# Kernel optimization log

Hardware: AMD Instinct MI355X
Metric: run time of the kernel (lower is better)

## Reference

```python
import jax, jax.numpy as jnp
import numpy as np

KERNEL_SIZE = 2
DILATION = 2


def aconv(x, A, shift):
    # x: [n, c, v, l], A: [v, w]; temporal roll + zero-mask first `shift` steps,
    # then node diffusion x . A over the node axis.
    xr = jnp.roll(x, shift, axis=3)
    if shift > 0:
        xr = xr.at[..., :shift].set(0.0)
    return jnp.einsum('ncvl,vw->ncwl', xr, A)


def setup_inputs() -> dict:
    key = jax.random.key(0)
    ks = jax.random.split(key, 7)
    N, C, V, L, E, CO = 32, 64, 500, 64, 10, 64
    return {
        'x': jax.random.normal(ks[0], (N, C, V, L), dtype=jnp.float32),
        'nodevec1': jax.random.normal(ks[1], (V, E), dtype=jnp.float32),
        'nodevec2': jax.random.normal(ks[2], (E, V), dtype=jnp.float32),
        'et_w': jax.random.normal(ks[3], (E, E), dtype=jnp.float32),
        'et_b': jax.random.normal(ks[4], (E,), dtype=jnp.float32),
        'mlp_w': jax.random.normal(ks[5], (CO, (1 + KERNEL_SIZE) * C), dtype=jnp.float32) * 0.05,
        'mlp_b': jax.random.normal(ks[6], (CO,), dtype=jnp.float32),
    }


def reference(x, nodevec1, nodevec2, et_w, et_b, mlp_w, mlp_b):
    out = [x]
    x2 = x
    shift = 0
    # hop 0: adaptive adjacency from node embeddings
    adp = jax.nn.softmax(jax.nn.relu(nodevec1 @ nodevec2), axis=1)
    x1 = aconv(x2, adp, shift)
    out.append(x1)
    shift = DILATION
    x2 = x1
    for i in range(KERNEL_SIZE - 1):
        # emb_trans: affine update of both node embeddings
        nodevec1 = nodevec1 @ et_w + et_b
        nodevec2 = (nodevec2.T @ et_w + et_b).T
        adp = jax.nn.softmax(jax.nn.relu(nodevec1 @ nodevec2), axis=1)
        x1 = aconv(x2, adp, shift)
        out.append(x1)
        shift = shift + DILATION
        x2 = x1
    h = jnp.concatenate(out, axis=1)  # [n, (1+K)*c, v, l]
    # 1x1 conv == channel matmul; dropout is identity at inference
    h = jnp.einsum('ncvl,oc->novl', h, mlp_w) + mlp_b[None, :, None, None]
    return h
```

## Files before the change

### kernel.cpp

```cpp
#include <hip/hip_runtime.h>
#include <hip/hip_bf16.h>

#define NB 32
#define CC 64
#define VV 500
#define LL 64
#define EE 10
#define CO 64
#define DIL 2
#define VP 512
#define SL (VV * LL)

typedef unsigned short u16;
typedef unsigned int   u32;
typedef __attribute__((ext_vector_type(8))) short bf16x8;
typedef __attribute__((ext_vector_type(4))) float f32x4;

typedef const __attribute__((address_space(1))) void g_void;
typedef __attribute__((address_space(3))) void l_void;

__device__ __forceinline__ float bf2f(u16 u) {
    union { u32 i; float f; } c; c.i = ((u32)u) << 16; return c.f;
}
__device__ __forceinline__ u16 f2bf(float f) {
    union { float f; u32 i; } c; c.f = f;
    u32 x = c.i;
    u32 r = (x + 0x7fffu + ((x >> 16) & 1u)) >> 16;
    return (u16)r;
}

__global__ void emb_kernel(const float* __restrict__ nv1, const float* __restrict__ nv2,
                           const float* __restrict__ et_w, const float* __restrict__ et_b,
                           const float* __restrict__ mlp_w,
                           float* __restrict__ nv1t, float* __restrict__ nv2t,
                           u16* __restrict__ wb) {
    int idx = blockIdx.x * blockDim.x + threadIdx.x;
    if (idx < VV * EE) {
        int v = idx / EE, e = idx - v * EE;
        float s = et_b[e];
        #pragma unroll
        for (int f = 0; f < EE; f++) s += nv1[v * EE + f] * et_w[f * EE + e];
        nv1t[idx] = s;
    } else if (idx < 2 * VV * EE) {
        int k = idx - VV * EE;
        int e = k / VV, v = k - e * VV;
        float s = et_b[e];
        #pragma unroll
        for (int f = 0; f < EE; f++) s += nv2[f * VV + v] * et_w[f * EE + e];
        nv2t[k] = s;
    } else if (idx < 2 * VV * EE + CO * 3 * CC) {
        int k = idx - 2 * VV * EE;
        wb[k] = f2bf(mlp_w[k]);
    }
}

__global__ __launch_bounds__(64) void adj_kernel(const float* __restrict__ p1,
                                                 const float* __restrict__ p2,
                                                 u16* __restrict__ Atb) {
    const int v = blockIdx.x;
    const int lane = threadIdx.x;
    if (v >= VV) {
        #pragma unroll
        for (int j = 0; j < 8; j++) Atb[(size_t)(lane + 64 * j) * VP + v] = 0;
        return;
    }
    float e1[EE];
    #pragma unroll
    for (int e = 0; e < EE; e++) e1[e] = p1[v * EE + e];

    float r[8];
    float m = -1e30f;
    #pragma unroll
    for (int j = 0; j < 8; j++) {
        int w = lane + 64 * j;
        if (w < VV) {
            float s = 0.f;
            #pragma unroll
            for (int e = 0; e < EE; e++) s += e1[e] * p2[e * VV + w];
            r[j] = fmaxf(s, 0.f);
            m = fmaxf(m, r[j]);
        } else {
            r[j] = -1e30f;
        }
    }
    #pragma unroll
    for (int off = 32; off > 0; off >>= 1) m = fmaxf(m, __shfl_xor(m, off));

    float p[8];
    float sum = 0.f;
    #pragma unroll
    for (int j = 0; j < 8; j++) {
        int w = lane + 64 * j;
        if (w < VV) { p[j] = expf(r[j] - m); sum += p[j]; }
    }
    #pragma unroll
    for (int off = 32; off > 0; off >>= 1) sum += __shfl_xor(sum, off);
    float inv = 1.f / sum;
    #pragma unroll
    for (int j = 0; j < 8; j++) {
        int w = lane + 64 * j;
        Atb[(size_t)w * VP + v] = (w < VV) ? f2bf(p[j] * inv) : (u16)0;
    }
}

__global__ __launch_bounds__(512, 2) void hops_fused(const float* __restrict__ x,
                                                     const u16* __restrict__ Atb0,
                                                     const u16* __restrict__ Atb1,
                                                     u16* __restrict__ x1g,
                                                     u16* __restrict__ x2g) {
    __shared__ u16 Xt[LL * VP];
    __shared__ u16 Ab[3][512 * 32];
    const int nc = blockIdx.x;
    const int tid = threadIdx.x;
    const size_t base = (size_t)nc * (VV * LL);
    const int lane = tid & 63;
    const int wv = tid >> 6;

    int ldsoff[4], rowoff[4];
    #pragma unroll
    for (int j = 0; j < 4; ++j) {
        const int lin = j * 8192 + tid * 16;
        const int w = lin >> 6;
        const int cell = ((lin >> 4) & 3) ^ ((w >> 1) & 3);
        ldsoff[j] = lin;
        rowoff[j] = w * VP + cell * 8;
    }
    char* abuf[3] = { (char*)&Ab[0][0], (char*)&Ab[1][0], (char*)&Ab[2][0] };

    auto issue_chunk = [&](const u16* Asrc, int kb, char* dst) {
        #pragma unroll
        for (int j = 0; j < 4; ++j)
            __builtin_amdgcn_global_load_lds(
                (g_void*)(Asrc + rowoff[j] + kb),
                (l_void*)(dst + ldsoff[j]), 16, 0, 0);
    };

    issue_chunk(Atb0, 0, abuf[0]);
    issue_chunk(Atb0, 32, abuf[1]);

    {
        char* ldsb = (char*)Xt;
        const int lquad = lane & 15;
        const int vsub = lane >> 4;
        const int l0 = 4 * lquad;
        #pragma unroll
        for (int i = 0; i < 8; ++i) {
            const int vp = wv * 32 + i * 4 + vsub;
            const int v0 = 2 * vp;
            u32 pk0, pk1, pk2, pk3;
            if (v0 < VV) {
                const float* xa = x + base + v0 * LL + l0;
                float4 fa = *(const float4*)xa;
                float4 fb = *(const float4*)(xa + LL);
                pk0 = (u32)f2bf(fa.x) | ((u32)f2bf(fb.x) << 16);
                pk1 = (u32)f2bf(fa.y) | ((u32)f2bf(fb.y) << 16);
                pk2 = (u32)f2bf(fa.z) | ((u32)f2bf(fb.z) << 16);
                pk3 = (u32)f2bf(fa.w) | ((u32)f2bf(fb.w) << 16);
            } else {
                pk0 = pk1 = pk2 = pk3 = 0;
            }
            const int vb = 4 * vp;
            int l = l0;
            *(u32*)(ldsb + l * (VP * 2) + (vb ^ ((l & 7) << 4))) = pk0; l++;
            *(u32*)(ldsb + l * (VP * 2) + (vb ^ ((l & 7) << 4))) = pk1; l++;
            *(u32*)(ldsb + l * (VP * 2) + (vb ^ ((l & 7) << 4))) = pk2; l++;
            *(u32*)(ldsb + l * (VP * 2) + (vb ^ ((l & 7) << 4))) = pk3;
        }
    }

    const int wr = wv * 64;
    const int r15 = lane & 15;
    const int kg = lane >> 4;
    const char* ldsb = (const char*)Xt;
    int lrow[4], lswz[4], aoff[4];
    #pragma unroll
    for (int ct = 0; ct < 4; ct++) {
        const int l = ct * 16 + r15;
        lrow[ct] = l * (VP * 2);
        lswz[ct] = (l & 7) << 4;
    }
    #pragma unroll
    for (int rt = 0; rt < 4; rt++) {
        const int w = wr + rt * 16 + r15;
        aoff[rt] = w * 64 + ((kg ^ ((w >> 1) & 3)) << 4);
    }

    f32x4 acc[4][4];
    #pragma unroll
    for (int rt = 0; rt < 4; rt++)
        #pragma unroll
        for (int ct = 0; ct < 4; ct++)
            acc[rt][ct] = (f32x4){0.f, 0.f, 0.f, 0.f};

    #pragma unroll
    for (int s = 0; s < 16; ++s) {
        asm volatile("s_waitcnt vmcnt(4) lgkmcnt(0)\n\ts_barrier" ::: "memory");
        const int g1 = s + 2;
        issue_chunk(g1 < 16 ? Atb0 : Atb1, (g1 & 15) * 32, abuf[g1 % 3]);

        const char* ac = abuf[s % 3];
        bf16x8 a[4], b[4];
        #pragma unroll
        for (int rt = 0; rt < 4; rt++)
            a[rt] = *(const bf16x8*)(ac + aoff[rt]);
        #pragma unroll
        for (int ct = 0; ct < 4; ct++)
            b[ct] = *(const bf16x8*)(ldsb + lrow[ct] + ((s * 64 + kg * 16) ^ lswz[ct]));
        #pragma unroll
        for (int rt = 0; rt < 4; rt++)
            #pragma unroll
            for (int ct = 0; ct < 4; ct++)
                acc[rt][ct] = __builtin_amdgcn_mfma_f32_16x16x32_bf16(a[rt], b[ct], acc[rt][ct], 0, 0, 0);
    }

    asm volatile("s_waitcnt vmcnt(0) lgkmcnt(0)\n\ts_barrier" ::: "memory");

    {
        u16* xo = x1g + base;
        #pragma unroll
        for (int rt = 0; rt < 4; rt++) {
            #pragma unroll
            for (int ct = 0; ct < 4; ct++) {
                const int col = ct * 16 + r15;
                const int wbase = wr + rt * 16 + kg * 4;
                f32x4 c = acc[rt][ct];
                #pragma unroll
                for (int r = 0; r < 4; r++) {
                    int w = wbase + r;
                    if (w < VV) xo[w * LL + col] = f2bf(c[r]);
                }
            }
        }
    }
    {
        char* ldsw = (char*)Xt;
        {
            const int l = tid >> 8;
            const int j = tid & 255;
            *(u32*)(ldsw + l * (VP * 2) + 4 * j) = 0;
        }
        #pragma unroll
        for (int rt = 0; rt < 4; rt++) {
            const int wb2 = (wr + rt * 16 + kg * 4) * 2;
            #pragma unroll
            for (int ct = 0; ct < 4; ct++) {
                const int col = ct * 16 + r15;
                const int ln = col + DIL;
                if (ln < LL) {
                    f32x4 c = acc[rt][ct];
                    u32 plo = (u32)f2bf(c[0]) | ((u32)f2bf(c[1]) << 16);
                    u32 phi = (u32)f2bf(c[2]) | ((u32)f2bf(c[3]) << 16);
                    const int swz = (ln & 7) << 4;
                    char* p = ldsw + ln * (VP * 2);
                    *(u32*)(p + (wb2 ^ swz)) = plo;
                    *(u32*)(p + ((wb2 + 4) ^ swz)) = phi;
                }
            }
        }
    }

    #pragma unroll
    for (int rt = 0; rt < 4; rt++)
        #pragma unroll
        for (int ct = 0; ct < 4; ct++)
            acc[rt][ct] = (f32x4){0.f, 0.f, 0.f, 0.f};

    #pragma unroll
    for (int s = 16; s < 32; ++s) {
        if (s <= 17) {
            asm volatile("s_waitcnt lgkmcnt(0)\n\ts_barrier" ::: "memory");
        } else {
            asm volatile("s_waitcnt vmcnt(4) lgkmcnt(0)\n\ts_barrier" ::: "memory");
        }
        const int g1 = s + 2;
        if (g1 < 32)
            issue_chunk(Atb1, (g1 & 15) * 32, abuf[g1 % 3]);

        const char* ac = abuf[s % 3];
        const int kk = s - 16;
        bf16x8 a[4], b[4];
        #pragma unroll
        for (int rt = 0; rt < 4; rt++)
            a[rt] = *(const bf16x8*)(ac + aoff[rt]);
        #pragma unroll
        for (int ct = 0; ct < 4; ct++)
            b[ct] = *(const bf16x8*)(ldsb + lrow[ct] + ((kk * 64 + kg * 16) ^ lswz[ct]));
        #pragma unroll
        for (int rt = 0; rt < 4; rt++)
            #pragma unroll
            for (int ct = 0; ct < 4; ct++)
                acc[rt][ct] = __builtin_amdgcn_mfma_f32_16x16x32_bf16(a[rt], b[ct], acc[rt][ct], 0, 0, 0);
    }

    {
        u16* xo = x2g + base;
        #pragma unroll
        for (int rt = 0; rt < 4; rt++) {
            #pragma unroll
            for (int ct = 0; ct < 4; ct++) {
                const int col = ct * 16 + r15;
                const int wbase = wr + rt * 16 + kg * 4;
                f32x4 c = acc[rt][ct];
                #pragma unroll
                for (int r = 0; r < 4; r++) {
                    int w = wbase + r;
                    if (w < VV) xo[w * LL + col] = f2bf(c[r]);
                }
            }
        }
    }
}

__global__ __launch_bounds__(256, 3) void mlp_mfma(const float* __restrict__ x,
                                                   const u16* __restrict__ x1,
                                                   const u16* __restrict__ x2,
                                                   const u16* __restrict__ wb,
                                                   const float* __restrict__ b,
                                                   float* __restrict__ out) {
    __shared__ u16 Ht[128 * 192];
    const int bid = blockIdx.x;
    const int n = bid / (SL / 128);
    const int st = bid - n * (SL / 128);
    const int s0 = st * 128;
    const int tid = threadIdx.x;

    const int lane = tid & 63;
    const int wv = tid >> 6;
    const int obase = (wv & 1) * 32;
    const int sbase = (wv >> 1) * 64;
    const int r15 = lane & 15;
    const int kg = lane >> 4;

    bf16x8 afrag[2][6];
    #pragma unroll
    for (int rt = 0; rt < 2; rt++)
        #pragma unroll
        for (int ks = 0; ks < 6; ks++)
            afrag[rt][ks] = *(const bf16x8*)(wb + (obase + rt * 16 + r15) * (3 * CC) + ks * 32 + kg * 8);

    {
        char* ldsb = (char*)Ht;
        const int squad = tid >> 3;
        const int pgroup = tid & 7;
        const int sq0 = 4 * squad;
        #pragma unroll
        for (int i = 0; i < 12; ++i) {
            const int P = i * 8 + pgroup;
            const int c = 2 * P;
            u32 pk0, pk1, pk2, pk3;
            if (i < 4) {
                const float* fsrc = x + ((size_t)n * CC + c) * SL + s0 + sq0;
                float4 va = *(const float4*)fsrc;
                float4 vb = *(const float4*)(fsrc + SL);
                pk0 = (u32)f2bf(va.x) | ((u32)f2bf(vb.x) << 16);
                pk1 = (u32)f2bf(va.y) | ((u32)f2bf(vb.y) << 16);
                pk2 = (u32)f2bf(va.z) | ((u32)f2bf(vb.z) << 16);
                pk3 = (u32)f2bf(va.w) | ((u32)f2bf(vb.w) << 16);
            } else {
                const u16* bsrc = (i < 8)
                    ? x1 + ((size_t)n * CC + (c - CC)) * SL + s0 + sq0
                    : x2 + ((size_t)n * CC + (c - 2 * CC)) * SL + s0 + sq0;
                uint2 va = *(const uint2*)bsrc;
                uint2 vb = *(const uint2*)(bsrc + SL);
                pk0 = (va.x & 0xffffu) | (vb.x << 16);
                pk1 = (va.x >> 16) | (vb.x & 0xffff0000u);
                pk2 = (va.y & 0xffffu) | (vb.y << 16);
                pk3 = (va.y >> 16) | (vb.y & 0xffff0000u);
            }
            int s = sq0;
            *(u32*)(ldsb + s * 384 + ((4 * P) ^ ((s & 7) << 4))) = pk0; s++;
            *(u32*)(ldsb + s * 384 + ((4 * P) ^ ((s & 7) << 4))) = pk1; s++;
            *(u32*)(ldsb + s * 384 + ((4 * P) ^ ((s & 7) << 4))) = pk2; s++;
            *(u32*)(ldsb + s * 384 + ((4 * P) ^ ((s & 7) << 4))) = pk3;
        }
    }
    __syncthreads();

    f32x4 acc[2][4];
    #pragma unroll
    for (int rt = 0; rt < 2; rt++)
        #pragma unroll
        for (int ct = 0; ct < 4; ct++)
            acc[rt][ct] = (f32x4){0.f, 0.f, 0.f, 0.f};

    const char* ldsb = (const char*)Ht;
    #pragma unroll
    for (int ks = 0; ks < 6; ks++) {
        bf16x8 bfr[4];
        #pragma unroll
        for (int ct = 0; ct < 4; ct++) {
            const int s = sbase + ct * 16 + r15;
            bfr[ct] = *(const bf16x8*)(ldsb + s * 384 + ((ks * 64 + kg * 16) ^ ((s & 7) << 4)));
        }
        #pragma unroll
        for (int rt = 0; rt < 2; rt++)
            #pragma unroll
            for (int ct = 0; ct < 4; ct++)
                acc[rt][ct] = __builtin_amdgcn_mfma_f32_16x16x32_bf16(afrag[rt][ks], bfr[ct], acc[rt][ct], 0, 0, 0);
    }

    #pragma unroll
    for (int rt = 0; rt < 2; rt++) {
        #pragma unroll
        for (int r = 0; r < 4; r++) {
            const int o = obase + rt * 16 + kg * 4 + r;
            const float bias = b[o];
            float* orow = out + ((size_t)n * CO + o) * SL + s0 + sbase;
            #pragma unroll
            for (int ct = 0; ct < 4; ct++)
                orow[ct * 16 + r15] = acc[rt][ct][r] + bias;
        }
    }
}

extern "C" void kernel_launch(void* const* d_in, const int* in_sizes, int n_in,
                              void* d_out, int out_size, void* d_ws, size_t ws_size,
                              hipStream_t stream) {
    const float* x     = (const float*)d_in[0];
    const float* nv1   = (const float*)d_in[1];
    const float* nv2   = (const float*)d_in[2];
    const float* et_w  = (const float*)d_in[3];
    const float* et_b  = (const float*)d_in[4];
    const float* mlp_w = (const float*)d_in[5];
    const float* mlp_b = (const float*)d_in[6];
    float* out = (float*)d_out;

    char* wsb = (char*)d_ws;
    size_t off = 0;
    auto alloc = [&](size_t bytes) {
        size_t o = off;
        off += (bytes + 255) & ~(size_t)255;
        return o;
    };
    u16*   Atb0 = (u16*)(wsb + alloc((size_t)VP * VP * 2));
    u16*   Atb1 = (u16*)(wsb + alloc((size_t)VP * VP * 2));
    float* nv1t = (float*)(wsb + alloc((size_t)VV * EE * 4));
    float* nv2t = (float*)(wsb + alloc((size_t)EE * VV * 4));
    u16*   wb   = (u16*)(wsb + alloc((size_t)CO * 3 * CC * 2));
    u16*   x1   = (u16*)(wsb + alloc((size_t)NB * CC * VV * LL * 2));
    u16*   x2   = (u16*)(wsb + alloc((size_t)NB * CC * VV * LL * 2));
    (void)in_sizes; (void)n_in; (void)out_size; (void)ws_size;

    const int embN = 2 * VV * EE + CO * 3 * CC;
    emb_kernel<<<(embN + 255) / 256, 256, 0, stream>>>(nv1, nv2, et_w, et_b, mlp_w, nv1t, nv2t, wb);
    adj_kernel<<<VP, 64, 0, stream>>>(nv1, nv2, Atb0);
    adj_kernel<<<VP, 64, 0, stream>>>(nv1t, nv2t, Atb1);
    hops_fused<<<NB * CC, 512, 0, stream>>>(x, Atb0, Atb1, x1, x2);
    mlp_mfma<<<NB * (SL / 128), 256, 0, stream>>>(x, x1, x2, wb, mlp_b, out);
}
```

Measured before the change: 462.8 us.

## Give each wave private A-tile buffers and drop per-step block barriers

Splits the shared triple-buffered adjacency tile into per-wave slices. Each wave now loads only its own 64 rows through global_load_lds, so the K-loop needs only a vmcnt wait and no s_barrier. Block-wide syncs stay only around the Xt rewrite between the two hops. The cost is wave-local waits and a different global access pattern per wave, with the same total LDS size.

```diff
diff --git a/kernel.cpp b/kernel.cpp
--- a/kernel.cpp
+++ b/kernel.cpp
@@ -109,34 +109,36 @@
                                                      u16* __restrict__ x1g,
                                                      u16* __restrict__ x2g) {
     __shared__ u16 Xt[LL * VP];
-    __shared__ u16 Ab[3][512 * 32];
+    __shared__ u16 Ab[8][3][64 * 32];
     const int nc = blockIdx.x;
     const int tid = threadIdx.x;
     const size_t base = (size_t)nc * (VV * LL);
     const int lane = tid & 63;
     const int wv = tid >> 6;
-
-    int ldsoff[4], rowoff[4];
+    const int wr = wv * 64;
+
+    int growoff[4];
     #pragma unroll
     for (int j = 0; j < 4; ++j) {
-        const int lin = j * 8192 + tid * 16;
-        const int w = lin >> 6;
-        const int cell = ((lin >> 4) & 3) ^ ((w >> 1) & 3);
-        ldsoff[j] = lin;
-        rowoff[j] = w * VP + cell * 8;
-    }
-    char* abuf[3] = { (char*)&Ab[0][0], (char*)&Ab[1][0], (char*)&Ab[2][0] };
+        const int lin = j * 1024 + lane * 16;
+        const int wl = lin >> 6;
+        const int cell = ((lin >> 4) & 3) ^ ((wl >> 1) & 3);
+        growoff[j] = (wr + wl) * VP + cell * 8;
+    }
+    char* mybuf[3];
+    #pragma unroll
+    for (int k = 0; k < 3; ++k) mybuf[k] = (char*)&Ab[wv][k][0];
 
     auto issue_chunk = [&](const u16* Asrc, int kb, char* dst) {
         #pragma unroll
         for (int j = 0; j < 4; ++j)
             __builtin_amdgcn_global_load_lds(
-                (g_void*)(Asrc + rowoff[j] + kb),
-                (l_void*)(dst + ldsoff[j]), 16, 0, 0);
+                (g_void*)(Asrc + growoff[j] + kb),
+                (l_void*)(dst + j * 1024 + lane * 16), 16, 0, 0);
     };
 
-    issue_chunk(Atb0, 0, abuf[0]);
-    issue_chunk(Atb0, 32, abuf[1]);
+    issue_chunk(Atb0, 0, mybuf[0]);
+    issue_chunk(Atb0, 32, mybuf[1]);
 
     {
         char* ldsb = (char*)Xt;
@@ -167,8 +169,8 @@
             *(u32*)(ldsb + l * (VP * 2) + (vb ^ ((l & 7) << 4))) = pk3;
         }
     }
-
-    const int wr = wv * 64;
+    __syncthreads();
+
     const int r15 = lane & 15;
     const int kg = lane >> 4;
     const char* ldsb = (const char*)Xt;
@@ -181,8 +183,8 @@
     }
     #pragma unroll
     for (int rt = 0; rt < 4; rt++) {
-        const int w = wr + rt * 16 + r15;
-        aoff[rt] = w * 64 + ((kg ^ ((w >> 1) & 3)) << 4);
+        const int wl = rt * 16 + r15;
+        aoff[rt] = wl * 64 + ((kg ^ ((wl >> 1) & 3)) << 4);
     }
 
     f32x4 acc[4][4];
@@ -194,11 +196,11 @@
 
     #pragma unroll
     for (int s = 0; s < 16; ++s) {
-        asm volatile("s_waitcnt vmcnt(4) lgkmcnt(0)\n\ts_barrier" ::: "memory");
+        asm volatile("s_waitcnt vmcnt(4) lgkmcnt(0)" ::: "memory");
         const int g1 = s + 2;
-        issue_chunk(g1 < 16 ? Atb0 : Atb1, (g1 & 15) * 32, abuf[g1 % 3]);
-
-        const char* ac = abuf[s % 3];
+        issue_chunk(g1 < 16 ? Atb0 : Atb1, (g1 & 15) * 32, mybuf[g1 % 3]);
+
+        const char* ac = mybuf[s % 3];
         bf16x8 a[4], b[4];
         #pragma unroll
         for (int rt = 0; rt < 4; rt++)
@@ -212,8 +214,6 @@
             for (int ct = 0; ct < 4; ct++)
                 acc[rt][ct] = __builtin_amdgcn_mfma_f32_16x16x32_bf16(a[rt], b[ct], acc[rt][ct], 0, 0, 0);
     }
-
-    asm volatile("s_waitcnt vmcnt(0) lgkmcnt(0)\n\ts_barrier" ::: "memory");
 
     {
         u16* xo = x1g + base;
@@ -232,6 +232,7 @@
             }
         }
     }
+    __syncthreads();
     {
         char* ldsw = (char*)Xt;
         {
@@ -258,6 +259,7 @@
             }
         }
     }
+    __syncthreads();
 
     #pragma unroll
     for (int rt = 0; rt < 4; rt++)
@@ -267,16 +269,16 @@
 
     #pragma unroll
     for (int s = 16; s < 32; ++s) {
-        if (s <= 17) {
-            asm volatile("s_waitcnt lgkmcnt(0)\n\ts_barrier" ::: "memory");
+        if (s == 31) {
+            asm volatile("s_waitcnt vmcnt(0) lgkmcnt(0)" ::: "memory");
         } else {
-            asm volatile("s_waitcnt vmcnt(4) lgkmcnt(0)\n\ts_barrier" ::: "memory");
+            asm volatile("s_waitcnt vmcnt(4) lgkmcnt(0)" ::: "memory");
         }
         const int g1 = s + 2;
         if (g1 < 32)
-            issue_chunk(Atb1, (g1 & 15) * 32, abuf[g1 % 3]);
-
-        const char* ac = abuf[s % 3];
+            issue_chunk(Atb1, (g1 & 15) * 32, mybuf[g1 % 3]);
+
+        const char* ac = mybuf[s % 3];
         const int kk = s - 16;
         bf16x8 a[4], b[4];
         #pragma unroll
```

After: 445.7 us. 3.7% less time.
